# Kernel tuning notes

Hardware: AMD Instinct MI355X
Metric: run time of the kernel (lower is better)

Reference implementation:

```python
import jax, jax.numpy as jnp
import numpy as np

N_NODES = 50000
N_EDGES = 800000
IN_DIM, HID_DIM, OUT_DIM = 128, 128, 64


def setup_inputs() -> dict:
    key = jax.random.key(0)
    ks = jax.random.split(key, 10)
    s = lambda d: 1.0 / np.sqrt(d)
    return {
        "feat": jax.random.normal(ks[0], (N_NODES, IN_DIM), jnp.float32),
        "W_self1": jax.random.normal(ks[1], (IN_DIM, HID_DIM), jnp.float32) * s(IN_DIM),
        "W_neigh1": jax.random.normal(ks[2], (IN_DIM, HID_DIM), jnp.float32) * s(IN_DIM),
        "b1": jnp.zeros((HID_DIM,), jnp.float32),
        "W_self2": jax.random.normal(ks[3], (HID_DIM, OUT_DIM), jnp.float32) * s(HID_DIM),
        "W_neigh2": jax.random.normal(ks[4], (HID_DIM, OUT_DIM), jnp.float32) * s(HID_DIM),
        "b2": jnp.zeros((OUT_DIM,), jnp.float32),
        "src": jax.random.randint(ks[5], (N_EDGES,), 0, N_NODES),
        "dst": jax.random.randint(ks[6], (N_EDGES,), 0, N_NODES),
        "neg_src": jax.random.randint(ks[7], (N_EDGES,), 0, N_NODES),
        "neg_dst": jax.random.randint(ks[8], (N_EDGES,), 0, N_NODES),
    }


def sage_conv(feat, src, dst, W_self, W_neigh, b):
    # DGL SAGEConv('mean'): out = feat @ W_self + mean_{u->v}(feat_u) @ W_neigh + b
    msg = feat[src]                                                      # [E, D] gather
    agg = jax.ops.segment_sum(msg, dst, num_segments=N_NODES)            # [N, D]
    deg = jax.ops.segment_sum(jnp.ones((src.shape[0], 1), feat.dtype), dst,
                              num_segments=N_NODES)                      # [N, 1]
    h_neigh = agg / jnp.maximum(deg, 1.0)                                # zero for isolated nodes
    return feat @ W_self + h_neigh @ W_neigh + b


def edge_dot(feat, src, dst):
    # dgl.function.u_dot_v -> [E, 1]
    return jnp.sum(feat[src] * feat[dst], axis=-1, keepdims=True)


def reference(feat, W_self1, W_neigh1, b1, W_self2, W_neigh2, b2,
              src, dst, neg_src, neg_dst):
    h = jax.nn.relu(sage_conv(feat, src, dst, W_self1, W_neigh1, b1))
    h = sage_conv(h, src, dst, W_self2, W_neigh2, b2)
    return (edge_dot(h, src, dst), edge_dot(h, neg_src, neg_dst))
```

## Files before the change

### kernel.cpp

```cpp
#include <hip/hip_runtime.h>

#define IN_DIM 128
#define HID_DIM 128
#define OUT_DIM 64

typedef short bf16x8 __attribute__((ext_vector_type(8)));
typedef float f32x4  __attribute__((ext_vector_type(4)));

__device__ inline float bflo(unsigned int u) { return __uint_as_float(u << 16); }
__device__ inline float bfhi(unsigned int u) { return __uint_as_float(u & 0xffff0000u); }
__device__ inline unsigned short f2bf(float f) {
    unsigned int b = __float_as_uint(f);
    return (unsigned short)((b + 0x7FFFu + ((b >> 16) & 1u)) >> 16);
}
__device__ inline unsigned int pack2(float a, float b) {
    return (unsigned int)f2bf(a) | ((unsigned int)f2bf(b) << 16);
}

__global__ void wtrans_kernel(const float* __restrict__ Ws1, const float* __restrict__ Wn1,
                              const float* __restrict__ Ws2, const float* __restrict__ Wn2,
                              unsigned short* __restrict__ Wt1, unsigned short* __restrict__ Wt2) {
    int tid = blockIdx.x * blockDim.x + threadIdx.x;
    if (tid < 4096) {
        int c = tid >> 4, k0 = (tid & 15) << 3;
        const float* W = (c < 128) ? (Ws1 + c) : (Wn1 + (c - 128));
        ushort4 a, b;
        a.x = f2bf(W[(size_t)(k0 + 0) * 128]); a.y = f2bf(W[(size_t)(k0 + 1) * 128]);
        a.z = f2bf(W[(size_t)(k0 + 2) * 128]); a.w = f2bf(W[(size_t)(k0 + 3) * 128]);
        b.x = f2bf(W[(size_t)(k0 + 4) * 128]); b.y = f2bf(W[(size_t)(k0 + 5) * 128]);
        b.z = f2bf(W[(size_t)(k0 + 6) * 128]); b.w = f2bf(W[(size_t)(k0 + 7) * 128]);
        *(ushort4*)&Wt1[c * 128 + k0]     = a;
        *(ushort4*)&Wt1[c * 128 + k0 + 4] = b;
    } else if (tid < 6144) {
        int t = tid - 4096;
        int c = t >> 4, k0 = (t & 15) << 3;
        const float* W = (c < 64) ? (Ws2 + c) : (Wn2 + (c - 64));
        ushort4 a, b;
        a.x = f2bf(W[(size_t)(k0 + 0) * 64]); a.y = f2bf(W[(size_t)(k0 + 1) * 64]);
        a.z = f2bf(W[(size_t)(k0 + 2) * 64]); a.w = f2bf(W[(size_t)(k0 + 3) * 64]);
        b.x = f2bf(W[(size_t)(k0 + 4) * 64]); b.y = f2bf(W[(size_t)(k0 + 5) * 64]);
        b.z = f2bf(W[(size_t)(k0 + 6) * 64]); b.w = f2bf(W[(size_t)(k0 + 7) * 64]);
        *(ushort4*)&Wt2[c * 128 + k0]     = a;
        *(ushort4*)&Wt2[c * 128 + k0 + 4] = b;
    }
}

__global__ void hist_rank_kernel(const int* __restrict__ dst, int* __restrict__ cnt,
                                 unsigned short* __restrict__ rank, int E) {
    int e = blockIdx.x * blockDim.x + threadIdx.x;
    if (e < E) rank[e] = (unsigned short)atomicAdd(&cnt[dst[e]], 1);
}

__global__ void block_sums_kernel(const int* __restrict__ cnt, int* __restrict__ partial, int N) {
    __shared__ int s[256];
    int i = blockIdx.x * 256 + threadIdx.x;
    s[threadIdx.x] = (i < N) ? cnt[i] : 0;
    __syncthreads();
    for (int o = 128; o > 0; o >>= 1) {
        if (threadIdx.x < o) s[threadIdx.x] += s[threadIdx.x + o];
        __syncthreads();
    }
    if (threadIdx.x == 0) partial[blockIdx.x] = s[0];
}

__global__ void scan_partials_kernel(int* __restrict__ partial, int nB) {
    __shared__ int s[256];
    int v = (threadIdx.x < nB) ? partial[threadIdx.x] : 0;
    s[threadIdx.x] = v;
    __syncthreads();
    for (int o = 1; o < 256; o <<= 1) {
        int t = (threadIdx.x >= o) ? s[threadIdx.x - o] : 0;
        __syncthreads();
        s[threadIdx.x] += t;
        __syncthreads();
    }
    if (threadIdx.x < nB) partial[threadIdx.x] = s[threadIdx.x] - v;
}

__global__ void scan_chunks_kernel(const int* __restrict__ cnt, const int* __restrict__ partial,
                                   int* __restrict__ row_ptr, int N) {
    __shared__ int s[256];
    int i = blockIdx.x * 256 + threadIdx.x;
    int v = (i < N) ? cnt[i] : 0;
    s[threadIdx.x] = v;
    __syncthreads();
    for (int o = 1; o < 256; o <<= 1) {
        int t = (threadIdx.x >= o) ? s[threadIdx.x - o] : 0;
        __syncthreads();
        s[threadIdx.x] += t;
        __syncthreads();
    }
    int incl = s[threadIdx.x];
    int base = partial[blockIdx.x];
    if (i < N) row_ptr[i] = base + incl - v;
    if (i == N - 1) row_ptr[N] = base + incl;
}

__global__ __launch_bounds__(256) void gemm1_fill_kernel(
        const float* __restrict__ x,
        const unsigned short* __restrict__ Wt,
        const float* __restrict__ bias,
        float* __restrict__ hs,
        unsigned short* __restrict__ t,
        int N, int FB,
        const int* __restrict__ src,
        const int* __restrict__ dst,
        const int* __restrict__ row_ptr,
        const unsigned short* __restrict__ rank,
        unsigned short* __restrict__ col_src,
        int E) {
    constexpr int DOUT = HID_DIM;
    constexpr int K   = 128;
    constexpr int MT  = 64;
    constexpr int SL  = 2 * DOUT / 4;
    constexpr int TN  = SL / 16;
    constexpr int TM  = MT / 16;
    constexpr int KS  = K / 32;
    constexpr int LDA = K + 8;

    __shared__ unsigned short sA[MT][LDA];

    const int tid = threadIdx.x;

    if ((int)blockIdx.x < FB) {
        int base = (int)blockIdx.x * 1024;
        #pragma unroll
        for (int k = 0; k < 4; ++k) {
            int e = base + k * 256 + tid;
            if (e < E) {
                int d = dst[e];
                col_src[row_ptr[d] + (int)rank[e]] = (unsigned short)src[e];
            }
        }
        return;
    }

    const int w   = tid >> 6;
    const int l   = tid & 63;
    const int l16 = l & 15;
    const int lhi = l >> 4;
    const int n0  = ((int)blockIdx.x - FB) * MT;

    #pragma unroll
    for (int it = 0; it < 8; ++it) {
        int flat = it * 256 + tid;
        int r  = flat >> 5;
        int c4 = flat & 31;
        float4 v = {0, 0, 0, 0};
        if (n0 + r < N) v = *(const float4*)&x[(size_t)(n0 + r) * K + c4 * 4];
        ushort4 p;
        p.x = f2bf(v.x); p.y = f2bf(v.y); p.z = f2bf(v.z); p.w = f2bf(v.w);
        *(ushort4*)&sA[r][c4 * 4] = p;
    }

    bf16x8 breg[TN][KS];
    float  bval[TN];
    #pragma unroll
    for (int tn = 0; tn < TN; ++tn) {
        const int c = w * SL + tn * 16 + l16;
        bval[tn] = (c < DOUT) ? bias[c] : 0.0f;
        #pragma unroll
        for (int ks = 0; ks < KS; ++ks)
            breg[tn][ks] = *(const bf16x8*)&Wt[c * 128 + ks * 32 + lhi * 8];
    }
    __syncthreads();

    f32x4 acc[TN][TM];
    #pragma unroll
    for (int tn = 0; tn < TN; ++tn)
        #pragma unroll
        for (int tm = 0; tm < TM; ++tm)
            acc[tn][tm] = (f32x4){0.0f, 0.0f, 0.0f, 0.0f};

    #pragma unroll
    for (int ks = 0; ks < KS; ++ks) {
        bf16x8 a[TM];
        #pragma unroll
        for (int tm = 0; tm < TM; ++tm)
            a[tm] = *(const bf16x8*)&sA[tm * 16 + l16][ks * 32 + lhi * 8];
        #pragma unroll
        for (int tn = 0; tn < TN; ++tn)
            #pragma unroll
            for (int tm = 0; tm < TM; ++tm)
                acc[tn][tm] = __builtin_amdgcn_mfma_f32_16x16x32_bf16(
                    a[tm], breg[tn][ks], acc[tn][tm], 0, 0, 0);
    }

    #pragma unroll
    for (int tn = 0; tn < TN; ++tn) {
        const int c = w * SL + tn * 16 + l16;
        const bool self = (c < DOUT);
        const int cc = self ? c : c - DOUT;
        #pragma unroll
        for (int tm = 0; tm < TM; ++tm) {
            #pragma unroll
            for (int r = 0; r < 4; ++r) {
                const int n = n0 + tm * 16 + lhi * 4 + r;
                if (n < N) {
                    const float v = acc[tn][tm][r] + bval[tn];
                    if (self) hs[(size_t)n * DOUT + cc] = v;
                    else      t [(size_t)n * DOUT + cc] = f2bf(v);
                }
            }
        }
    }
}

__global__ void gather_mean128_kernel(const unsigned short* __restrict__ t,
                                      const float* __restrict__ base,
                                      const int* __restrict__ row_ptr,
                                      const unsigned short* __restrict__ col_src,
                                      unsigned short* __restrict__ out, int N) {
    int node = (blockIdx.x * blockDim.x + threadIdx.x) >> 6;
    int lane = threadIdx.x & 63;
    if (node >= N) return;
    const int beg = row_ptr[node], end = row_ptr[node + 1];
    const float rdeg = 1.0f / fmaxf((float)(end - beg), 1.0f);
    const int off = lane * 2;

    float a0x = 0, a0y = 0, a1x = 0, a1y = 0, a2x = 0, a2y = 0, a3x = 0, a3y = 0;
    int i = beg;
    for (; i + 4 <= end; i += 4) {
        int s0 = col_src[i], s1 = col_src[i + 1], s2 = col_src[i + 2], s3 = col_src[i + 3];
        unsigned int u0 = *(const unsigned int*)&t[(size_t)s0 * 128 + off];
        unsigned int u1 = *(const unsigned int*)&t[(size_t)s1 * 128 + off];
        unsigned int u2 = *(const unsigned int*)&t[(size_t)s2 * 128 + off];
        unsigned int u3 = *(const unsigned int*)&t[(size_t)s3 * 128 + off];
        a0x += bflo(u0); a0y += bfhi(u0);
        a1x += bflo(u1); a1y += bfhi(u1);
        a2x += bflo(u2); a2y += bfhi(u2);
        a3x += bflo(u3); a3y += bfhi(u3);
    }
    for (; i < end; ++i) {
        unsigned int u = *(const unsigned int*)&t[(size_t)col_src[i] * 128 + off];
        a0x += bflo(u); a0y += bfhi(u);
    }
    float ax = (a0x + a1x) + (a2x + a3x);
    float ay = (a0y + a1y) + (a2y + a3y);
    float2 b = *(const float2*)&base[(size_t)node * 128 + off];
    float ox = fmaxf(b.x + ax * rdeg, 0.0f);
    float oy = fmaxf(b.y + ay * rdeg, 0.0f);
    *(unsigned int*)&out[(size_t)node * 128 + off] = pack2(ox, oy);
}

__global__ __launch_bounds__(256) void gemm2_kernel(
        const unsigned short* __restrict__ x,
        const unsigned short* __restrict__ Wt,
        const float* __restrict__ bias,
        float* __restrict__ hs2,
        unsigned short* __restrict__ t2,
        int N) {
    constexpr int DOUT = OUT_DIM;
    constexpr int K   = 128;
    constexpr int MT  = 64;
    constexpr int SL  = 2 * DOUT / 4;
    constexpr int TN  = SL / 16;
    constexpr int TM  = MT / 16;
    constexpr int KS  = K / 32;
    constexpr int LDA = K + 8;

    __shared__ unsigned short sA[MT][LDA];

    const int tid = threadIdx.x;
    const int w   = tid >> 6;
    const int l   = tid & 63;
    const int l16 = l & 15;
    const int lhi = l >> 4;
    const int n0  = (int)blockIdx.x * MT;

    #pragma unroll
    for (int it = 0; it < 4; ++it) {
        int flat = it * 256 + tid;
        int r  = flat >> 4;
        int c8 = flat & 15;
        uint4 v = {0, 0, 0, 0};
        if (n0 + r < N) v = *(const uint4*)&x[(size_t)(n0 + r) * K + c8 * 8];
        *(uint4*)&sA[r][c8 * 8] = v;
    }

    bf16x8 breg[TN][KS];
    float  bval[TN];
    #pragma unroll
    for (int tn = 0; tn < TN; ++tn) {
        const int c = w * SL + tn * 16 + l16;
        bval[tn] = (c < DOUT) ? bias[c] : 0.0f;
        #pragma unroll
        for (int ks = 0; ks < KS; ++ks)
            breg[tn][ks] = *(const bf16x8*)&Wt[c * 128 + ks * 32 + lhi * 8];
    }
    __syncthreads();

    f32x4 acc[TN][TM];
    #pragma unroll
    for (int tn = 0; tn < TN; ++tn)
        #pragma unroll
        for (int tm = 0; tm < TM; ++tm)
            acc[tn][tm] = (f32x4){0.0f, 0.0f, 0.0f, 0.0f};

    #pragma unroll
    for (int ks = 0; ks < KS; ++ks) {
        bf16x8 a[TM];
        #pragma unroll
        for (int tm = 0; tm < TM; ++tm)
            a[tm] = *(const bf16x8*)&sA[tm * 16 + l16][ks * 32 + lhi * 8];
        #pragma unroll
        for (int tn = 0; tn < TN; ++tn)
            #pragma unroll
            for (int tm = 0; tm < TM; ++tm)
                acc[tn][tm] = __builtin_amdgcn_mfma_f32_16x16x32_bf16(
                    a[tm], breg[tn][ks], acc[tn][tm], 0, 0, 0);
    }

    #pragma unroll
    for (int tn = 0; tn < TN; ++tn) {
        const int c = w * SL + tn * 16 + l16;
        const bool self = (c < DOUT);
        const int cc = self ? c : c - DOUT;
        #pragma unroll
        for (int tm = 0; tm < TM; ++tm) {
            #pragma unroll
            for (int r = 0; r < 4; ++r) {
                const int n = n0 + tm * 16 + lhi * 4 + r;
                if (n < N) {
                    const float v = acc[tn][tm][r] + bval[tn];
                    if (self) hs2[(size_t)n * DOUT + cc] = v;
                    else      t2 [(size_t)n * DOUT + cc] = f2bf(v);
                }
            }
        }
    }
}

__global__ void gather_mean64_kernel(const unsigned short* __restrict__ t,
                                     const float* __restrict__ base,
                                     const int* __restrict__ row_ptr,
                                     const unsigned short* __restrict__ col_src,
                                     unsigned short* __restrict__ out, int N) {
    int tid  = blockIdx.x * blockDim.x + threadIdx.x;
    int node = (tid >> 6) * 2 + ((tid >> 5) & 1);
    int m    = tid & 31;
    if (node >= N) return;
    const int beg = row_ptr[node], end = row_ptr[node + 1];
    const float rdeg = 1.0f / fmaxf((float)(end - beg), 1.0f);
    const int off = m * 2;

    float a0x = 0, a0y = 0, a1x = 0, a1y = 0, a2x = 0, a2y = 0, a3x = 0, a3y = 0;
    int i = beg;
    for (; i + 4 <= end; i += 4) {
        int s0 = col_src[i], s1 = col_src[i + 1], s2 = col_src[i + 2], s3 = col_src[i + 3];
        unsigned int u0 = *(const unsigned int*)&t[(size_t)s0 * 64 + off];
        unsigned int u1 = *(const unsigned int*)&t[(size_t)s1 * 64 + off];
        unsigned int u2 = *(const unsigned int*)&t[(size_t)s2 * 64 + off];
        unsigned int u3 = *(const unsigned int*)&t[(size_t)s3 * 64 + off];
        a0x += bflo(u0); a0y += bfhi(u0);
        a1x += bflo(u1); a1y += bfhi(u1);
        a2x += bflo(u2); a2y += bfhi(u2);
        a3x += bflo(u3); a3y += bfhi(u3);
    }
    for (; i < end; ++i) {
        unsigned int u = *(const unsigned int*)&t[(size_t)col_src[i] * 64 + off];
        a0x += bflo(u); a0y += bfhi(u);
    }
    float ax = (a0x + a1x) + (a2x + a3x);
    float ay = (a0y + a1y) + (a2y + a3y);
    float2 b = *(const float2*)&base[(size_t)node * 64 + off];
    *(unsigned int*)&out[(size_t)node * 64 + off] = pack2(b.x + ax * rdeg, b.y + ay * rdeg);
}

__global__ void edge_dot_kernel(const unsigned short* __restrict__ h,
                                const int* __restrict__ src,
                                const int* __restrict__ dst,
                                const int* __restrict__ nsrc,
                                const int* __restrict__ ndst,
                                float* __restrict__ out,
                                int E) {
    int tid = blockIdx.x * blockDim.x + threadIdx.x;
    int eg = tid >> 3;
    int l  = tid & 7;
    if (eg >= 2 * E) return;
    int s, t;
    if (eg < E) { s = src[eg];      t = dst[eg]; }
    else        { s = nsrc[eg - E]; t = ndst[eg - E]; }
    const uint4 a = *reinterpret_cast<const uint4*>(&h[(size_t)s * OUT_DIM + l * 8]);
    const uint4 b = *reinterpret_cast<const uint4*>(&h[(size_t)t * OUT_DIM + l * 8]);
    float v = bflo(a.x) * bflo(b.x) + bfhi(a.x) * bfhi(b.x)
            + bflo(a.y) * bflo(b.y) + bfhi(a.y) * bfhi(b.y)
            + bflo(a.z) * bflo(b.z) + bfhi(a.z) * bfhi(b.z)
            + bflo(a.w) * bflo(b.w) + bfhi(a.w) * bfhi(b.w);
    v += __shfl_xor(v, 4, 8);
    v += __shfl_xor(v, 2, 8);
    v += __shfl_xor(v, 1, 8);
    if (l == 0) out[eg] = v;
}

extern "C" void kernel_launch(void* const* d_in, const int* in_sizes, int n_in,
                              void* d_out, int out_size, void* d_ws, size_t ws_size,
                              hipStream_t stream) {
    const float* feat = (const float*)d_in[0];
    const float* Ws1  = (const float*)d_in[1];
    const float* Wn1  = (const float*)d_in[2];
    const float* b1   = (const float*)d_in[3];
    const float* Ws2  = (const float*)d_in[4];
    const float* Wn2  = (const float*)d_in[5];
    const float* b2   = (const float*)d_in[6];
    const int* src  = (const int*)d_in[7];
    const int* dst  = (const int*)d_in[8];
    const int* nsrc = (const int*)d_in[9];
    const int* ndst = (const int*)d_in[10];
    const int E = in_sizes[7];
    const int N = in_sizes[0] / IN_DIM;
    const int NB = (N + 255) / 256;
    const int NT = (N + 63) / 64;
    const int FB = (E + 1023) / 1024;

    char* wsb = (char*)d_ws;
    unsigned short* Wt1 = (unsigned short*)wsb;
    unsigned short* Wt2 = Wt1 + 256 * 128;
    unsigned short* t1  = Wt2 + 128 * 128;
    float* hs1          = (float*)(t1 + (size_t)N * HID_DIM);
    unsigned short* h1  = (unsigned short*)(hs1 + (size_t)N * HID_DIM);
    unsigned short* t2  = h1 + (size_t)N * HID_DIM;
    float* hs2          = (float*)(t2 + (size_t)N * OUT_DIM);
    unsigned short* h2  = (unsigned short*)(hs2 + (size_t)N * OUT_DIM);
    int* cnt            = (int*)(h2 + (size_t)N * OUT_DIM);
    int* row_ptr        = cnt + N;
    int* partial        = row_ptr + N + 1;
    unsigned short* rank    = (unsigned short*)(partial + 256);
    unsigned short* col_src = rank + E;

    wtrans_kernel<<<24, 256, 0, stream>>>(Ws1, Wn1, Ws2, Wn2, Wt1, Wt2);

    hipMemsetAsync(cnt, 0, sizeof(int) * (size_t)N, stream);
    hist_rank_kernel<<<(E + 255) / 256, 256, 0, stream>>>(dst, cnt, rank, E);
    block_sums_kernel<<<NB, 256, 0, stream>>>(cnt, partial, N);
    scan_partials_kernel<<<1, 256, 0, stream>>>(partial, NB);
    scan_chunks_kernel<<<NB, 256, 0, stream>>>(cnt, partial, row_ptr, N);

    gemm1_fill_kernel<<<FB + NT, 256, 0, stream>>>(
        feat, Wt1, b1, hs1, t1, N, FB,
        src, dst, row_ptr, rank, col_src, E);

    gather_mean128_kernel<<<(N * 64 + 255) / 256, 256, 0, stream>>>(
        t1, hs1, row_ptr, col_src, h1, N);

    gemm2_kernel<<<NT, 256, 0, stream>>>(
        h1, Wt2, b2, hs2, t2, N);

    {
        int waves = (N + 1) / 2;
        gather_mean64_kernel<<<(waves * 64 + 255) / 256, 256, 0, stream>>>(
            t2, hs2, row_ptr, col_src, h2, N);
    }

    {
        int total = 2 * E * 8;
        edge_dot_kernel<<<(total + 255) / 256, 256, 0, stream>>>(
            h2, src, dst, nsrc, ndst, (float*)d_out, E);
    }
}
```

Baseline: 197.9 us.

## Fuse prep kernels, store self-term in bf16, and widen edge-dot lanes

Merges the weight transpose into the histogram kernel and folds the partial-scan kernel into the chunk scan, where each block now reduces its preceding partials itself. This removes two launches. The self-projection intermediates (hs1, hs2) are now stored in bf16 instead of fp32, halving their write and read traffic in the GEMM and gather kernels at some precision cost. The edge-dot kernel uses 4 lanes per edge with two 16-byte loads each instead of 8 lanes, cutting thread count and shuffle steps.

```diff
diff --git a/kernel.cpp b/kernel.cpp
--- a/kernel.cpp
+++ b/kernel.cpp
@@ -16,38 +16,45 @@
 __device__ inline unsigned int pack2(float a, float b) {
     return (unsigned int)f2bf(a) | ((unsigned int)f2bf(b) << 16);
 }
-
-__global__ void wtrans_kernel(const float* __restrict__ Ws1, const float* __restrict__ Wn1,
-                              const float* __restrict__ Ws2, const float* __restrict__ Wn2,
-                              unsigned short* __restrict__ Wt1, unsigned short* __restrict__ Wt2) {
-    int tid = blockIdx.x * blockDim.x + threadIdx.x;
-    if (tid < 4096) {
-        int c = tid >> 4, k0 = (tid & 15) << 3;
-        const float* W = (c < 128) ? (Ws1 + c) : (Wn1 + (c - 128));
-        ushort4 a, b;
-        a.x = f2bf(W[(size_t)(k0 + 0) * 128]); a.y = f2bf(W[(size_t)(k0 + 1) * 128]);
-        a.z = f2bf(W[(size_t)(k0 + 2) * 128]); a.w = f2bf(W[(size_t)(k0 + 3) * 128]);
-        b.x = f2bf(W[(size_t)(k0 + 4) * 128]); b.y = f2bf(W[(size_t)(k0 + 5) * 128]);
-        b.z = f2bf(W[(size_t)(k0 + 6) * 128]); b.w = f2bf(W[(size_t)(k0 + 7) * 128]);
-        *(ushort4*)&Wt1[c * 128 + k0]     = a;
-        *(ushort4*)&Wt1[c * 128 + k0 + 4] = b;
-    } else if (tid < 6144) {
-        int t = tid - 4096;
-        int c = t >> 4, k0 = (t & 15) << 3;
-        const float* W = (c < 64) ? (Ws2 + c) : (Wn2 + (c - 64));
-        ushort4 a, b;
-        a.x = f2bf(W[(size_t)(k0 + 0) * 64]); a.y = f2bf(W[(size_t)(k0 + 1) * 64]);
-        a.z = f2bf(W[(size_t)(k0 + 2) * 64]); a.w = f2bf(W[(size_t)(k0 + 3) * 64]);
-        b.x = f2bf(W[(size_t)(k0 + 4) * 64]); b.y = f2bf(W[(size_t)(k0 + 5) * 64]);
-        b.z = f2bf(W[(size_t)(k0 + 6) * 64]); b.w = f2bf(W[(size_t)(k0 + 7) * 64]);
-        *(ushort4*)&Wt2[c * 128 + k0]     = a;
-        *(ushort4*)&Wt2[c * 128 + k0 + 4] = b;
-    }
-}
-
-__global__ void hist_rank_kernel(const int* __restrict__ dst, int* __restrict__ cnt,
-                                 unsigned short* __restrict__ rank, int E) {
-    int e = blockIdx.x * blockDim.x + threadIdx.x;
+__device__ inline float dot8(uint4 a, uint4 b) {
+    return bflo(a.x) * bflo(b.x) + bfhi(a.x) * bfhi(b.x)
+         + bflo(a.y) * bflo(b.y) + bfhi(a.y) * bfhi(b.y)
+         + bflo(a.z) * bflo(b.z) + bfhi(a.z) * bfhi(b.z)
+         + bflo(a.w) * bflo(b.w) + bfhi(a.w) * bfhi(b.w);
+}
+
+__global__ void wtrans_hist_kernel(const float* __restrict__ Ws1, const float* __restrict__ Wn1,
+                                   const float* __restrict__ Ws2, const float* __restrict__ Wn2,
+                                   unsigned short* __restrict__ Wt1, unsigned short* __restrict__ Wt2,
+                                   const int* __restrict__ dst, int* __restrict__ cnt,
+                                   unsigned short* __restrict__ rank, int E) {
+    if ((int)blockIdx.x < 24) {
+        int tid = (int)blockIdx.x * 256 + threadIdx.x;
+        if (tid < 4096) {
+            int c = tid >> 4, k0 = (tid & 15) << 3;
+            const float* W = (c < 128) ? (Ws1 + c) : (Wn1 + (c - 128));
+            ushort4 a, b;
+            a.x = f2bf(W[(size_t)(k0 + 0) * 128]); a.y = f2bf(W[(size_t)(k0 + 1) * 128]);
+            a.z = f2bf(W[(size_t)(k0 + 2) * 128]); a.w = f2bf(W[(size_t)(k0 + 3) * 128]);
+            b.x = f2bf(W[(size_t)(k0 + 4) * 128]); b.y = f2bf(W[(size_t)(k0 + 5) * 128]);
+            b.z = f2bf(W[(size_t)(k0 + 6) * 128]); b.w = f2bf(W[(size_t)(k0 + 7) * 128]);
+            *(ushort4*)&Wt1[c * 128 + k0]     = a;
+            *(ushort4*)&Wt1[c * 128 + k0 + 4] = b;
+        } else if (tid < 6144) {
+            int t = tid - 4096;
+            int c = t >> 4, k0 = (t & 15) << 3;
+            const float* W = (c < 64) ? (Ws2 + c) : (Wn2 + (c - 64));
+            ushort4 a, b;
+            a.x = f2bf(W[(size_t)(k0 + 0) * 64]); a.y = f2bf(W[(size_t)(k0 + 1) * 64]);
+            a.z = f2bf(W[(size_t)(k0 + 2) * 64]); a.w = f2bf(W[(size_t)(k0 + 3) * 64]);
+            b.x = f2bf(W[(size_t)(k0 + 4) * 64]); b.y = f2bf(W[(size_t)(k0 + 5) * 64]);
+            b.z = f2bf(W[(size_t)(k0 + 6) * 64]); b.w = f2bf(W[(size_t)(k0 + 7) * 64]);
+            *(ushort4*)&Wt2[c * 128 + k0]     = a;
+            *(ushort4*)&Wt2[c * 128 + k0 + 4] = b;
+        }
+        return;
+    }
+    int e = ((int)blockIdx.x - 24) * 256 + threadIdx.x;
     if (e < E) rank[e] = (unsigned short)atomicAdd(&cnt[dst[e]], 1);
 }
 
@@ -63,35 +70,29 @@
     if (threadIdx.x == 0) partial[blockIdx.x] = s[0];
 }
 
-__global__ void scan_partials_kernel(int* __restrict__ partial, int nB) {
+__global__ void scan_chunks_kernel(const int* __restrict__ cnt, const int* __restrict__ partial,
+                                   int* __restrict__ row_ptr, int N, int NB) {
     __shared__ int s[256];
-    int v = (threadIdx.x < nB) ? partial[threadIdx.x] : 0;
-    s[threadIdx.x] = v;
+    const int t = threadIdx.x;
+    s[t] = (t < NB && t < (int)blockIdx.x) ? partial[t] : 0;
+    __syncthreads();
+    for (int o = 128; o > 0; o >>= 1) {
+        if (t < o) s[t] += s[t + o];
+        __syncthreads();
+    }
+    const int base = s[0];
+    __syncthreads();
+    int i = blockIdx.x * 256 + t;
+    int v = (i < N) ? cnt[i] : 0;
+    s[t] = v;
     __syncthreads();
     for (int o = 1; o < 256; o <<= 1) {
-        int t = (threadIdx.x >= o) ? s[threadIdx.x - o] : 0;
+        int tv = (t >= o) ? s[t - o] : 0;
         __syncthreads();
-        s[threadIdx.x] += t;
+        s[t] += tv;
         __syncthreads();
     }
-    if (threadIdx.x < nB) partial[threadIdx.x] = s[threadIdx.x] - v;
-}
-
-__global__ void scan_chunks_kernel(const int* __restrict__ cnt, const int* __restrict__ partial,
-                                   int* __restrict__ row_ptr, int N) {
-    __shared__ int s[256];
-    int i = blockIdx.x * 256 + threadIdx.x;
-    int v = (i < N) ? cnt[i] : 0;
-    s[threadIdx.x] = v;
-    __syncthreads();
-    for (int o = 1; o < 256; o <<= 1) {
-        int t = (threadIdx.x >= o) ? s[threadIdx.x - o] : 0;
-        __syncthreads();
-        s[threadIdx.x] += t;
-        __syncthreads();
-    }
-    int incl = s[threadIdx.x];
-    int base = partial[blockIdx.x];
+    int incl = s[t];
     if (i < N) row_ptr[i] = base + incl - v;
     if (i == N - 1) row_ptr[N] = base + incl;
 }
@@ -100,7 +101,7 @@
         const float* __restrict__ x,
         const unsigned short* __restrict__ Wt,
         const float* __restrict__ bias,
-        float* __restrict__ hs,
+        unsigned short* __restrict__ hsb,
         unsigned short* __restrict__ t,
         int N, int FB,
         const int* __restrict__ src,
@@ -197,9 +198,9 @@
             for (int r = 0; r < 4; ++r) {
                 const int n = n0 + tm * 16 + lhi * 4 + r;
                 if (n < N) {
-                    const float v = acc[tn][tm][r] + bval[tn];
-                    if (self) hs[(size_t)n * DOUT + cc] = v;
-                    else      t [(size_t)n * DOUT + cc] = f2bf(v);
+                    const unsigned short v = f2bf(acc[tn][tm][r] + bval[tn]);
+                    if (self) hsb[(size_t)n * DOUT + cc] = v;
+                    else      t  [(size_t)n * DOUT + cc] = v;
                 }
             }
         }
@@ -207,7 +208,7 @@
 }
 
 __global__ void gather_mean128_kernel(const unsigned short* __restrict__ t,
-                                      const float* __restrict__ base,
+                                      const unsigned short* __restrict__ base,
                                       const int* __restrict__ row_ptr,
                                       const unsigned short* __restrict__ col_src,
                                       unsigned short* __restrict__ out, int N) {
@@ -237,9 +238,9 @@
     }
     float ax = (a0x + a1x) + (a2x + a3x);
     float ay = (a0y + a1y) + (a2y + a3y);
-    float2 b = *(const float2*)&base[(size_t)node * 128 + off];
-    float ox = fmaxf(b.x + ax * rdeg, 0.0f);
-    float oy = fmaxf(b.y + ay * rdeg, 0.0f);
+    unsigned int ub = *(const unsigned int*)&base[(size_t)node * 128 + off];
+    float ox = fmaxf(bflo(ub) + ax * rdeg, 0.0f);
+    float oy = fmaxf(bfhi(ub) + ay * rdeg, 0.0f);
     *(unsigned int*)&out[(size_t)node * 128 + off] = pack2(ox, oy);
 }
 
@@ -247,7 +248,7 @@
         const unsigned short* __restrict__ x,
         const unsigned short* __restrict__ Wt,
         const float* __restrict__ bias,
-        float* __restrict__ hs2,
+        unsigned short* __restrict__ hsb2,
         unsigned short* __restrict__ t2,
         int N) {
     constexpr int DOUT = OUT_DIM;
@@ -322,9 +323,9 @@
             for (int r = 0; r < 4; ++r) {
                 const int n = n0 + tm * 16 + lhi * 4 + r;
                 if (n < N) {
-                    const float v = acc[tn][tm][r] + bval[tn];
-                    if (self) hs2[(size_t)n * DOUT + cc] = v;
-                    else      t2 [(size_t)n * DOUT + cc] = f2bf(v);
+                    const unsigned short v = f2bf(acc[tn][tm][r] + bval[tn]);
+                    if (self) hsb2[(size_t)n * DOUT + cc] = v;
+                    else      t2  [(size_t)n * DOUT + cc] = v;
                 }
             }
         }
@@ -332,7 +333,7 @@
 }
 
 __global__ void gather_mean64_kernel(const unsigned short* __restrict__ t,
-                                     const float* __restrict__ base,
+                                     const unsigned short* __restrict__ base,
                                      const int* __restrict__ row_ptr,
                                      const unsigned short* __restrict__ col_src,
                                      unsigned short* __restrict__ out, int N) {
@@ -363,8 +364,9 @@
     }
     float ax = (a0x + a1x) + (a2x + a3x);
     float ay = (a0y + a1y) + (a2y + a3y);
-    float2 b = *(const float2*)&base[(size_t)node * 64 + off];
-    *(unsigned int*)&out[(size_t)node * 64 + off] = pack2(b.x + ax * rdeg, b.y + ay * rdeg);
+    unsigned int ub = *(const unsigned int*)&base[(size_t)node * 64 + off];
+    *(unsigned int*)&out[(size_t)node * 64 + off] =
+        pack2(bflo(ub) + ax * rdeg, bfhi(ub) + ay * rdeg);
 }
 
 __global__ void edge_dot_kernel(const unsigned short* __restrict__ h,
@@ -375,21 +377,19 @@
                                 float* __restrict__ out,
                                 int E) {
     int tid = blockIdx.x * blockDim.x + threadIdx.x;
-    int eg = tid >> 3;
-    int l  = tid & 7;
+    int eg = tid >> 2;
+    int l  = tid & 3;
     if (eg >= 2 * E) return;
     int s, t;
     if (eg < E) { s = src[eg];      t = dst[eg]; }
     else        { s = nsrc[eg - E]; t = ndst[eg - E]; }
-    const uint4 a = *reinterpret_cast<const uint4*>(&h[(size_t)s * OUT_DIM + l * 8]);
-    const uint4 b = *reinterpret_cast<const uint4*>(&h[(size_t)t * OUT_DIM + l * 8]);
-    float v = bflo(a.x) * bflo(b.x) + bfhi(a.x) * bfhi(b.x)
-            + bflo(a.y) * bflo(b.y) + bfhi(a.y) * bfhi(b.y)
-            + bflo(a.z) * bflo(b.z) + bfhi(a.z) * bfhi(b.z)
-            + bflo(a.w) * bflo(b.w) + bfhi(a.w) * bfhi(b.w);
-    v += __shfl_xor(v, 4, 8);
-    v += __shfl_xor(v, 2, 8);
-    v += __shfl_xor(v, 1, 8);
+    const uint4* pa = (const uint4*)&h[(size_t)s * OUT_DIM + l * 16];
+    const uint4* pb = (const uint4*)&h[(size_t)t * OUT_DIM + l * 16];
+    uint4 a0 = pa[0], a1 = pa[1];
+    uint4 b0 = pb[0], b1 = pb[1];
+    float v = dot8(a0, b0) + dot8(a1, b1);
+    v += __shfl_xor(v, 2, 4);
+    v += __shfl_xor(v, 1, 4);
     if (l == 0) out[eg] = v;
 }
 
@@ -412,48 +412,47 @@
     const int NB = (N + 255) / 256;
     const int NT = (N + 63) / 64;
     const int FB = (E + 1023) / 1024;
+    const int HB = (E + 255) / 256;
 
     char* wsb = (char*)d_ws;
-    unsigned short* Wt1 = (unsigned short*)wsb;
-    unsigned short* Wt2 = Wt1 + 256 * 128;
-    unsigned short* t1  = Wt2 + 128 * 128;
-    float* hs1          = (float*)(t1 + (size_t)N * HID_DIM);
-    unsigned short* h1  = (unsigned short*)(hs1 + (size_t)N * HID_DIM);
-    unsigned short* t2  = h1 + (size_t)N * HID_DIM;
-    float* hs2          = (float*)(t2 + (size_t)N * OUT_DIM);
-    unsigned short* h2  = (unsigned short*)(hs2 + (size_t)N * OUT_DIM);
-    int* cnt            = (int*)(h2 + (size_t)N * OUT_DIM);
-    int* row_ptr        = cnt + N;
-    int* partial        = row_ptr + N + 1;
+    unsigned short* Wt1  = (unsigned short*)wsb;
+    unsigned short* Wt2  = Wt1 + 256 * 128;
+    unsigned short* t1   = Wt2 + 128 * 128;
+    unsigned short* hs1b = t1 + (size_t)N * HID_DIM;
+    unsigned short* h1   = hs1b + (size_t)N * HID_DIM;
+    unsigned short* t2   = h1 + (size_t)N * HID_DIM;
+    unsigned short* hs2b = t2 + (size_t)N * OUT_DIM;
+    unsigned short* h2   = hs2b + (size_t)N * OUT_DIM;
+    int* cnt             = (int*)(h2 + (size_t)N * OUT_DIM);
+    int* row_ptr         = cnt + N;
+    int* partial         = row_ptr + N + 1;
     unsigned short* rank    = (unsigned short*)(partial + 256);
     unsigned short* col_src = rank + E;
 
-    wtrans_kernel<<<24, 256, 0, stream>>>(Ws1, Wn1, Ws2, Wn2, Wt1, Wt2);
-
     hipMemsetAsync(cnt, 0, sizeof(int) * (size_t)N, stream);
-    hist_rank_kernel<<<(E + 255) / 256, 256, 0, stream>>>(dst, cnt, rank, E);
+    wtrans_hist_kernel<<<24 + HB, 256, 0, stream>>>(
+        Ws1, Wn1, Ws2, Wn2, Wt1, Wt2, dst, cnt, rank, E);
     block_sums_kernel<<<NB, 256, 0, stream>>>(cnt, partial, N);
-    scan_partials_kernel<<<1, 256, 0, stream>>>(partial, NB);
-    scan_chunks_kernel<<<NB, 256, 0, stream>>>(cnt, partial, row_ptr, N);
+    scan_chunks_kernel<<<NB, 256, 0, stream>>>(cnt, partial, row_ptr, N, NB);
 
     gemm1_fill_kernel<<<FB + NT, 256, 0, stream>>>(
-        feat, Wt1, b1, hs1, t1, N, FB,
+        feat, Wt1, b1, hs1b, t1, N, FB,
         src, dst, row_ptr, rank, col_src, E);
 
     gather_mean128_kernel<<<(N * 64 + 255) / 256, 256, 0, stream>>>(
-        t1, hs1, row_ptr, col_src, h1, N);
+        t1, hs1b, row_ptr, col_src, h1, N);
 
     gemm2_kernel<<<NT, 256, 0, stream>>>(
-        h1, Wt2, b2, hs2, t2, N);
+        h1, Wt2, b2, hs2b, t2, N);
 
     {
         int waves = (N + 1) / 2;
         gather_mean64_kernel<<<(waves * 64 + 255) / 256, 256, 0, stream>>>(
-            t2, hs2, row_ptr, col_src, h2, N);
+            t2, hs2b, row_ptr, col_src, h2, N);
     }
 
     {
-        int total = 2 * E * 8;
+        int total = 2 * E * 4;
         edge_dot_kernel<<<(total + 255) / 256, 256, 0, stream>>>(
             h2, src, dst, nsrc, ndst, (float*)d_out, E);
     }
```

Measured after the change: 183.6 us. 1.08x faster.
